# Kernel tuning notes

Hardware: AMD Instinct MI355X
Metric: run time of the kernel (lower is better)

Reference implementation:

```python
import jax, jax.numpy as jnp
import numpy as np

B, SEQ, C_IN, F, K = 32, 16384, 64, 64, 9

def setup_inputs() -> dict:
    key = jax.random.key(0)
    k1, k2 = jax.random.split(key)
    x = jax.random.normal(k1, (B, SEQ, C_IN), dtype=jnp.float32)
    w = jax.random.normal(k2, (F, K, C_IN), dtype=jnp.float32) * 0.05  # mimics random_normal_initializer stddev
    b = jnp.zeros((F,), dtype=jnp.float32)
    return {"x": x, "w": w, "b": b}

def reference(x, w, b):
    # Faithful math: out[bt, t, f] = sum_{k,c} w[f,k,c] * x[bt, t+k, c] + b[f]
    # (VALID padding, stride 1). Expressed as an efficient conv instead of the
    # original unrolled loop + giant stacked intermediate.
    kernel = jnp.transpose(w, (1, 2, 0))  # [K, C_in, F] for WIO layout
    out = jax.lax.conv_general_dilated(
        x, kernel,
        window_strides=(1,),
        padding='VALID',
        dimension_numbers=('NWC', 'WIO', 'NWC'),
    )  # [B, SEQ-K+1, F]
    return out + b[None, None, :]
```

## Files before the change

kernel.cpp:

```cpp
#include <hip/hip_runtime.h>
#include <hip/hip_bf16.h>

#define T_IN   16384
#define T_OUT  16376
#define CIN    64
#define NF     64
#define KT     9
#define NB     32
#define TILE   128
#define ROWS   (TILE + KT - 1)
#define LDS_STRIDE 72
#define TILES_PER_BATCH 128
#define NTILES (NB * TILES_PER_BATCH)
#define NBLOCKS 512
#define TILE_ITERS (NTILES / NBLOCKS)

typedef __bf16 bf16x8 __attribute__((ext_vector_type(8)));
typedef unsigned short u16x8 __attribute__((ext_vector_type(8)));
typedef unsigned short u16x4 __attribute__((ext_vector_type(4)));
typedef float f32x16 __attribute__((ext_vector_type(16)));

__device__ __forceinline__ unsigned short f2bf(float f) {
    unsigned u = __builtin_bit_cast(unsigned, f);
    u += 0x7FFFu + ((u >> 16) & 1u);
    return (unsigned short)(u >> 16);
}

__global__ __launch_bounds__(256, 2) void conv1d_mfma_kernel(
    const float* __restrict__ x,
    const float* __restrict__ w,
    const float* __restrict__ b,
    float* __restrict__ out)
{
    __shared__ __attribute__((aligned(16))) unsigned short ldsX[ROWS * LDS_STRIDE];

    const int tid  = threadIdx.x;
    const int lane = tid & 63;
    const int wv   = tid >> 6;
    const int half = lane >> 5;
    const int l31  = lane & 31;
    const int fh   = wv & 1;
    const int rh   = wv >> 1;
    const int fbase = fh * 32;
    const int rbase = rh * 64;
    const int fcol  = fbase + l31;

    bf16x8 Bf[KT][4];
#pragma unroll
    for (int k = 0; k < KT; ++k) {
#pragma unroll
        for (int s = 0; s < 4; ++s) {
            const float* wp = w + (size_t)fcol * (KT * CIN) + k * CIN + s * 16 + half * 8;
            const float4 w0 = *(const float4*)(wp);
            const float4 w1 = *(const float4*)(wp + 4);
            u16x8 t;
            t[0] = f2bf(w0.x); t[1] = f2bf(w0.y); t[2] = f2bf(w0.z); t[3] = f2bf(w0.w);
            t[4] = f2bf(w1.x); t[5] = f2bf(w1.y); t[6] = f2bf(w1.z); t[7] = f2bf(w1.w);
            Bf[k][s] = __builtin_bit_cast(bf16x8, t);
        }
    }
    const float bias = b[fcol];

    for (int it = 0; it < TILE_ITERS; ++it) {
        const int g  = blockIdx.x * TILE_ITERS + it;
        const int bb = g >> 7;
        const int t0 = (g & 127) << 7;

        for (int i = tid; i < ROWS * 16; i += 256) {
            const int r  = i >> 4;
            const int cg = i & 15;
            int gr = t0 + r;
            gr = gr < (T_IN - 1) ? gr : (T_IN - 1);
            const float4 v = *(const float4*)(x + ((size_t)bb * T_IN + gr) * CIN + cg * 4);
            u16x4 p;
            p[0] = f2bf(v.x); p[1] = f2bf(v.y); p[2] = f2bf(v.z); p[3] = f2bf(v.w);
            *(u16x4*)&ldsX[r * LDS_STRIDE + cg * 4] = p;
        }
        __syncthreads();

        f32x16 acc0 = {0,0,0,0,0,0,0,0,0,0,0,0,0,0,0,0};
        f32x16 acc1 = {0,0,0,0,0,0,0,0,0,0,0,0,0,0,0,0};
        const int abase = (rbase + l31) * LDS_STRIDE + half * 8;
#pragma unroll
        for (int k = 0; k < KT; ++k) {
#pragma unroll
            for (int s = 0; s < 4; ++s) {
                const int off = abase + k * LDS_STRIDE + s * 16;
                bf16x8 a0 = *(const bf16x8*)&ldsX[off];
                bf16x8 a1 = *(const bf16x8*)&ldsX[off + 32 * LDS_STRIDE];
                acc0 = __builtin_amdgcn_mfma_f32_32x32x16_bf16(a0, Bf[k][s], acc0, 0, 0, 0);
                acc1 = __builtin_amdgcn_mfma_f32_32x32x16_bf16(a1, Bf[k][s], acc1, 0, 0, 0);
            }
        }

#pragma unroll
        for (int m = 0; m < 2; ++m) {
            const f32x16 A = m ? acc1 : acc0;
#pragma unroll
            for (int r = 0; r < 16; ++r) {
                const int tl = rbase + m * 32 + (r & 3) + 8 * (r >> 2) + 4 * half;
                const int tg = t0 + tl;
                if (tg < T_OUT)
                    out[((size_t)bb * T_OUT + tg) * NF + fcol] = A[r] + bias;
            }
        }
        __syncthreads();
    }
}

extern "C" void kernel_launch(void* const* d_in, const int* in_sizes, int n_in,
                              void* d_out, int out_size, void* d_ws, size_t ws_size,
                              hipStream_t stream) {
    const float* x = (const float*)d_in[0];
    const float* w = (const float*)d_in[1];
    const float* b = (const float*)d_in[2];
    float* out = (float*)d_out;
    conv1d_mfma_kernel<<<NBLOCKS, 256, 0, stream>>>(x, w, b, out);
}
```

Before: 295.0 us.

## Pre-convert input to planar bf16 and double-buffer tiles via async LDS loads

Adds a pre-pass kernel that converts x from fp32 to bf16 in a workspace buffer, laid out in planes of 8 channels. The conv kernel then fills LDS with direct global-to-LDS async loads into two alternating buffers, so the next tile loads while MFMA runs on the current one. This aims to remove per-tile conversion work and hide load latency. The cost is an extra pass over the input that writes and then rereads a 64 MB bf16 copy. If the workspace is too small, a fallback path runs the original kernel.

New measurement: 318.6 us. 8.0% more time.

```diff
diff --git a/kernel.cpp b/kernel.cpp
--- a/kernel.cpp
+++ b/kernel.cpp
@@ -8,12 +8,13 @@
 #define KT     9
 #define NB     32
 #define TILE   128
-#define ROWS   (TILE + KT - 1)
-#define LDS_STRIDE 72
-#define TILES_PER_BATCH 128
-#define NTILES (NB * TILES_PER_BATCH)
+#define ROWS   136
+#define CGS    8
+#define PLANE  (ROWS * 8)
 #define NBLOCKS 512
-#define TILE_ITERS (NTILES / NBLOCKS)
+#define TILE_ITERS 8
+#define WS_SHORTS ((size_t)NB * T_IN * CIN)
+#define WS_BYTES  (WS_SHORTS * 2)
 
 typedef __bf16 bf16x8 __attribute__((ext_vector_type(8)));
 typedef unsigned short u16x8 __attribute__((ext_vector_type(8)));
@@ -26,13 +27,40 @@
     return (unsigned short)(u >> 16);
 }
 
-__global__ __launch_bounds__(256, 2) void conv1d_mfma_kernel(
-    const float* __restrict__ x,
+__device__ __forceinline__ void async_load16(const unsigned short* g, unsigned short* l) {
+    __builtin_amdgcn_global_load_lds(
+        (const __attribute__((address_space(1))) void*)g,
+        (__attribute__((address_space(3))) void*)l, 16, 0, 0);
+}
+
+__global__ __launch_bounds__(256) void convert_bf16_kernel(
+    const float* __restrict__ x, unsigned short* __restrict__ ws)
+{
+    const int tid = blockIdx.x * 256 + threadIdx.x;
+#pragma unroll
+    for (int i = 0; i < 8; ++i) {
+        const int idx = tid + i * 524288;
+        const int bb  = idx >> 17;
+        const int rem = idx & 131071;
+        const int t   = rem >> 3;
+        const int cg  = rem & 7;
+        const float* xp = x + ((size_t)bb * T_IN + t) * CIN + cg * 8;
+        const float4 v0 = *(const float4*)xp;
+        const float4 v1 = *(const float4*)(xp + 4);
+        u16x8 p;
+        p[0] = f2bf(v0.x); p[1] = f2bf(v0.y); p[2] = f2bf(v0.z); p[3] = f2bf(v0.w);
+        p[4] = f2bf(v1.x); p[5] = f2bf(v1.y); p[6] = f2bf(v1.z); p[7] = f2bf(v1.w);
+        *(u16x8*)&ws[((size_t)(bb * CGS + cg) * T_IN + t) * 8] = p;
+    }
+}
+
+__global__ __launch_bounds__(256, 2) void conv1d_mfma_dma_kernel(
+    const unsigned short* __restrict__ xb,
     const float* __restrict__ w,
     const float* __restrict__ b,
     float* __restrict__ out)
 {
-    __shared__ __attribute__((aligned(16))) unsigned short ldsX[ROWS * LDS_STRIDE];
+    __shared__ __attribute__((aligned(16))) unsigned short ldsX[2][CGS * PLANE];
 
     const int tid  = threadIdx.x;
     const int lane = tid & 63;
@@ -41,9 +69,8 @@
     const int l31  = lane & 31;
     const int fh   = wv & 1;
     const int rh   = wv >> 1;
-    const int fbase = fh * 32;
     const int rbase = rh * 64;
-    const int fcol  = fbase + l31;
+    const int fcol  = fh * 32 + l31;
 
     bf16x8 Bf[KT][4];
 #pragma unroll
@@ -61,11 +88,99 @@
     }
     const float bias = b[fcol];
 
+    const int base = blockIdx.x * TILE_ITERS;
+
+    auto stage = [&](int g, int d) {
+        const int bb = g >> 7;
+        const int t0 = (g & 127) << 7;
+        for (int j = wv; j < 24; j += 4) {
+            const int cg = j / 3;
+            const int p  = j - cg * 3;
+            const int r0 = (p == 0) ? 0 : (p == 1) ? 64 : 72;
+            int gr = t0 + r0 + lane;
+            gr = gr < T_IN ? gr : (T_IN - 1);
+            const unsigned short* gp = xb + ((size_t)(bb * CGS + cg) * T_IN + gr) * 8;
+            async_load16(gp, &ldsX[d][(cg * ROWS + r0) * 8]);
+        }
+    };
+
+    stage(base, 0);
+    __syncthreads();
+
+    for (int it = 0; it < TILE_ITERS; ++it) {
+        const int g  = base + it;
+        const int bb = g >> 7;
+        const int t0 = (g & 127) << 7;
+        const int c  = it & 1;
+        const bool more = (it + 1 < TILE_ITERS);
+
+        if (more) stage(g + 1, c ^ 1);
+
+        f32x16 acc0 = {0,0,0,0,0,0,0,0,0,0,0,0,0,0,0,0};
+        f32x16 acc1 = {0,0,0,0,0,0,0,0,0,0,0,0,0,0,0,0};
+        const unsigned short* lx = &ldsX[c][half * PLANE + (rbase + l31) * 8];
+#pragma unroll
+        for (int k = 0; k < KT; ++k) {
+#pragma unroll
+            for (int s = 0; s < 4; ++s) {
+                const int off = s * (2 * PLANE) + k * 8;
+                bf16x8 a0 = *(const bf16x8*)&lx[off];
+                bf16x8 a1 = *(const bf16x8*)&lx[off + 256];
+                acc0 = __builtin_amdgcn_mfma_f32_32x32x16_bf16(a0, Bf[k][s], acc0, 0, 0, 0);
+                acc1 = __builtin_amdgcn_mfma_f32_32x32x16_bf16(a1, Bf[k][s], acc1, 0, 0, 0);
+            }
+        }
+
+#pragma unroll
+        for (int m = 0; m < 2; ++m) {
+            const f32x16 A = m ? acc1 : acc0;
+#pragma unroll
+            for (int r = 0; r < 16; ++r) {
+                const int tl = rbase + m * 32 + (r & 3) + 8 * (r >> 2) + 4 * half;
+                const int tg = t0 + tl;
+                if (tg < T_OUT)
+                    out[((size_t)bb * T_OUT + tg) * NF + fcol] = A[r] + bias;
+            }
+        }
+
+        __syncthreads();
+    }
+}
+
+#define LDS_STRIDE 72
+__global__ __launch_bounds__(256, 2) void conv1d_fallback(
+    const float* __restrict__ x, const float* __restrict__ w,
+    const float* __restrict__ b, float* __restrict__ out)
+{
+    __shared__ __attribute__((aligned(16))) unsigned short ldsF[ROWS * LDS_STRIDE];
+    const int tid  = threadIdx.x;
+    const int lane = tid & 63;
+    const int wv   = tid >> 6;
+    const int half = lane >> 5;
+    const int l31  = lane & 31;
+    const int rbase = (wv >> 1) * 64;
+    const int fcol  = (wv & 1) * 32 + l31;
+
+    bf16x8 Bf[KT][4];
+#pragma unroll
+    for (int k = 0; k < KT; ++k) {
+#pragma unroll
+        for (int s = 0; s < 4; ++s) {
+            const float* wp = w + (size_t)fcol * (KT * CIN) + k * CIN + s * 16 + half * 8;
+            const float4 w0 = *(const float4*)(wp);
+            const float4 w1 = *(const float4*)(wp + 4);
+            u16x8 t;
+            t[0] = f2bf(w0.x); t[1] = f2bf(w0.y); t[2] = f2bf(w0.z); t[3] = f2bf(w0.w);
+            t[4] = f2bf(w1.x); t[5] = f2bf(w1.y); t[6] = f2bf(w1.z); t[7] = f2bf(w1.w);
+            Bf[k][s] = __builtin_bit_cast(bf16x8, t);
+        }
+    }
+    const float bias = b[fcol];
+
     for (int it = 0; it < TILE_ITERS; ++it) {
         const int g  = blockIdx.x * TILE_ITERS + it;
         const int bb = g >> 7;
         const int t0 = (g & 127) << 7;
-
         for (int i = tid; i < ROWS * 16; i += 256) {
             const int r  = i >> 4;
             const int cg = i & 15;
@@ -74,10 +189,9 @@
             const float4 v = *(const float4*)(x + ((size_t)bb * T_IN + gr) * CIN + cg * 4);
             u16x4 p;
             p[0] = f2bf(v.x); p[1] = f2bf(v.y); p[2] = f2bf(v.z); p[3] = f2bf(v.w);
-            *(u16x4*)&ldsX[r * LDS_STRIDE + cg * 4] = p;
+            *(u16x4*)&ldsF[r * LDS_STRIDE + cg * 4] = p;
         }
         __syncthreads();
-
         f32x16 acc0 = {0,0,0,0,0,0,0,0,0,0,0,0,0,0,0,0};
         f32x16 acc1 = {0,0,0,0,0,0,0,0,0,0,0,0,0,0,0,0};
         const int abase = (rbase + l31) * LDS_STRIDE + half * 8;
@@ -86,13 +200,12 @@
 #pragma unroll
             for (int s = 0; s < 4; ++s) {
                 const int off = abase + k * LDS_STRIDE + s * 16;
-                bf16x8 a0 = *(const bf16x8*)&ldsX[off];
-                bf16x8 a1 = *(const bf16x8*)&ldsX[off + 32 * LDS_STRIDE];
+                bf16x8 a0 = *(const bf16x8*)&ldsF[off];
+                bf16x8 a1 = *(const bf16x8*)&ldsF[off + 32 * LDS_STRIDE];
                 acc0 = __builtin_amdgcn_mfma_f32_32x32x16_bf16(a0, Bf[k][s], acc0, 0, 0, 0);
                 acc1 = __builtin_amdgcn_mfma_f32_32x32x16_bf16(a1, Bf[k][s], acc1, 0, 0, 0);
             }
         }
-
 #pragma unroll
         for (int m = 0; m < 2; ++m) {
             const f32x16 A = m ? acc1 : acc0;
@@ -115,5 +228,11 @@
     const float* w = (const float*)d_in[1];
     const float* b = (const float*)d_in[2];
     float* out = (float*)d_out;
-    conv1d_mfma_kernel<<<NBLOCKS, 256, 0, stream>>>(x, w, b, out);
-}
+    if (ws_size >= WS_BYTES && d_ws != nullptr) {
+        unsigned short* ws = (unsigned short*)d_ws;
+        convert_bf16_kernel<<<2048, 256, 0, stream>>>(x, ws);
+        conv1d_mfma_dma_kernel<<<NBLOCKS, 256, 0, stream>>>(ws, w, b, out);
+    } else {
+        conv1d_fallback<<<NBLOCKS, 256, 0, stream>>>(x, w, b, out);
+    }
+}
```
